# Kernel optimization log

Hardware: AMD Instinct MI355X
Metric: run time of the kernel (lower is better)

The kernel has to match this reference:

```python
import jax, jax.numpy as jnp
import numpy as np

N = 100000      # nodes
E = 3200000     # edges (avg degree 32)
IN_CH = 32
EDGE_DIM = 11
HID = IN_CH + 4 + EDGE_DIM   # 47
OUT = 128


def setup_inputs() -> dict:
    key = jax.random.key(0)
    ks = jax.random.split(key, 10)
    x = jax.random.normal(ks[0], (N, IN_CH), dtype=jnp.float32)
    pos = jax.random.normal(ks[1], (N, 3), dtype=jnp.float32) * 10.0
    nrm = jax.random.normal(ks[2], (N, 3), dtype=jnp.float32)
    normal = nrm / jnp.linalg.norm(nrm, axis=1, keepdims=True)
    # edges with src != dst (avoids degenerate zero-distance point pairs)
    src = jax.random.randint(ks[3], (E,), 0, N)
    off = jax.random.randint(ks[4], (E,), 1, N)
    dst = (src + off) % N
    edge_index = jnp.stack([src, dst], axis=0).astype(jnp.int64)
    edge_attr = jax.random.normal(ks[5], (E, EDGE_DIM), dtype=jnp.float32)
    W1 = jax.random.normal(ks[6], (HID, HID), dtype=jnp.float32) / np.sqrt(HID)
    b1 = jnp.zeros((HID,), dtype=jnp.float32)
    g1 = jnp.ones((HID,), dtype=jnp.float32)
    be1 = jnp.zeros((HID,), dtype=jnp.float32)
    W2 = jax.random.normal(ks[7], (HID, OUT), dtype=jnp.float32) / np.sqrt(HID)
    b2 = jnp.zeros((OUT,), dtype=jnp.float32)
    g2 = jnp.ones((OUT,), dtype=jnp.float32)
    be2 = jnp.zeros((OUT,), dtype=jnp.float32)
    return {"x": x, "pos": pos, "normal": normal, "edge_attr": edge_attr,
            "W1": W1, "b1": b1, "g1": g1, "be1": be1,
            "W2": W2, "b2": b2, "g2": g2, "be2": be2,
            "edge_index": edge_index}


def _angle(v1, v2):
    return jnp.arctan2(jnp.linalg.norm(jnp.cross(v1, v2), axis=1),
                       jnp.sum(v1 * v2, axis=1))


def _layernorm(h, g, b, eps=1e-5):
    mu = jnp.mean(h, axis=-1, keepdims=True)
    var = jnp.var(h, axis=-1, keepdims=True)  # biased, matches torch LayerNorm
    return (h - mu) / jnp.sqrt(var + eps) * g + b


def reference(x, pos, normal, edge_attr, W1, b1, g1, be1, W2, b2, g2, be2, edge_index):
    src, dst = edge_index[0], edge_index[1]  # message flows src(j) -> dst(i)
    pos_i, pos_j = pos[dst], pos[src]
    n_i, n_j = normal[dst], normal[src]
    x_j = x[src]
    pseudo = pos_j - pos_i                                  # [E,3]
    ppf = jnp.stack([jnp.linalg.norm(pseudo, axis=1),
                     _angle(n_i, pseudo),
                     _angle(n_j, pseudo),
                     _angle(n_i, n_j)], axis=1)             # [E,4]
    msg = jnp.concatenate([x_j, ppf, edge_attr], axis=1)    # [E,47]
    # local_nn = MLP([47,47,128]): (Lin->ReLU->LayerNorm->Dropout(eval)) x2
    h = _layernorm(jax.nn.relu(msg @ W1 + b1), g1, be1)     # [E,47]
    h = _layernorm(jax.nn.relu(h @ W2 + b2), g2, be2)       # [E,128]
    out = jax.ops.segment_max(h, dst, num_segments=N)       # scatter-max per target node
    return jnp.where(jnp.isfinite(out), out, 0.0)           # nodes w/o edges -> 0
```

## Files before the change

kernel.cpp:

```cpp
#include <hip/hip_runtime.h>
#include <cstdint>
#include <cstddef>


typedef _Float16 f16x8 __attribute__((ext_vector_type(8)));
typedef _Float16 f16x2 __attribute__((ext_vector_type(2)));
typedef float    f32x4 __attribute__((ext_vector_type(4)));

#define ENC_NEGINF 0x007FFFFFu
#define LDK 64
#define LDH 132

__device__ __forceinline__ int swz(int row, int col) {
    return (col & 7) | ((((col >> 3) ^ row) & 7) << 3);
}

__device__ __forceinline__ unsigned fenc(float f) {
    unsigned u = __float_as_uint(f);
    return (u & 0x80000000u) ? ~u : (u | 0x80000000u);
}

__device__ __forceinline__ float fdec(unsigned k) {
    if (k == ENC_NEGINF) return 0.0f;
    unsigned u = (k & 0x80000000u) ? (k ^ 0x80000000u) : ~k;
    return __uint_as_float(u);
}

__device__ __forceinline__ f16x2 pkrtz(float a, float b) {
    auto p = __builtin_amdgcn_cvt_pkrtz(a, b);
    return __builtin_bit_cast(f16x2, p);
}

__global__ void init_out_kernel(unsigned* __restrict__ out, int n4) {
    int i = blockIdx.x * blockDim.x + threadIdx.x;
    if (i < n4)
        ((uint4*)out)[i] = make_uint4(ENC_NEGINF, ENC_NEGINF, ENC_NEGINF, ENC_NEGINF);
}

__global__ void finalize_out_kernel(float* __restrict__ out, int n4) {
    int i = blockIdx.x * blockDim.x + threadIdx.x;
    if (i < n4) {
        uint4 k = ((const uint4*)out)[i];
        float4 r;
        r.x = fdec(k.x); r.y = fdec(k.y); r.z = fdec(k.z); r.w = fdec(k.w);
        ((float4*)out)[i] = r;
    }
}

__global__ void hist_kernel(const int* __restrict__ dstI, int* __restrict__ counts, int E) {
    int i = blockIdx.x * blockDim.x + threadIdx.x;
    if (i < E) atomicAdd(&counts[dstI[i]], 1);
}

__global__ __launch_bounds__(1024) void scan_blk(const int* __restrict__ in,
                                                 int* __restrict__ outp,
                                                 int* __restrict__ bsums, int N) {
    __shared__ int wsum[16];
    const int tid = threadIdx.x, lane = tid & 63, wid = tid >> 6;
    int i = blockIdx.x * 1024 + tid;
    int v = (i < N) ? in[i] : 0;
    int incl = v;
#pragma unroll
    for (int m = 1; m < 64; m <<= 1) {
        int t = __shfl_up(incl, m, 64);
        if (lane >= m) incl += t;
    }
    if (lane == 63) wsum[wid] = incl;
    __syncthreads();
    int woff = 0;
#pragma unroll
    for (int k = 0; k < 16; ++k) woff += (k < wid) ? wsum[k] : 0;
    if (i < N) outp[i] = woff + incl - v;
    if (tid == 1023 && bsums != nullptr) bsums[blockIdx.x] = woff + incl;
}

__global__ void scatter_kernel(const int* __restrict__ srcI, const int* __restrict__ dstI,
                               int* __restrict__ nextp, const int* __restrict__ bsums,
                               int2* __restrict__ se, int* __restrict__ dst_g, int E) {
    int i = blockIdx.x * blockDim.x + threadIdx.x;
    if (i < E) {
        int d = dstI[i];
        int p = bsums[d >> 10] + atomicAdd(&nextp[d], 1);
        se[p] = make_int2(srcI[i], i);
        dst_g[p] = d;
    }
}

__global__ __launch_bounds__(512, 4) void edge_kernel_csr(
    const float* __restrict__ x,   const float* __restrict__ pos,
    const float* __restrict__ nrm, const float* __restrict__ ea,
    const float* __restrict__ W1,  const float* __restrict__ b1,
    const float* __restrict__ g1,  const float* __restrict__ be1,
    const float* __restrict__ W2,  const float* __restrict__ b2,
    const float* __restrict__ g2,  const float* __restrict__ be2,
    const int2* __restrict__ se,   const int* __restrict__ dst_g,
    unsigned* __restrict__ out, int E, int ntiles, int tilesPerBlock)
{
    __shared__ _Float16 W1t[48][LDK];
    __shared__ _Float16 W2t[128][LDK];
    __shared__ _Float16 msgA[128][LDK];
    __shared__ _Float16 h2w[128][LDH];
    __shared__ int dstL[128];

    const int lane = threadIdx.x & 63;
    const int w    = threadIdx.x >> 6;
    const int c16  = lane & 15;
    const int g    = lane >> 4;
    const int row0 = w * 16;

    for (int i = threadIdx.x; i < 48 * 64; i += 512) {
        int n = i >> 6, k = i & 63;
        W1t[n][swz(n, k)] = (n < 47 && k < 47) ? (_Float16)W1[k * 47 + n] : (_Float16)0.f;
    }
    for (int i = threadIdx.x; i < 128 * 64; i += 512) {
        int n = i >> 6, k = i & 63;
        W2t[n][swz(n, k)] = (k < 47) ? (_Float16)W2[k * 128 + n] : (_Float16)0.f;
    }
    for (int i = threadIdx.x; i < 128 * LDK; i += 512)
        (&msgA[0][0])[i] = (_Float16)0.f;

    float b1v[3], g1v[3], be1v[3];
#pragma unroll
    for (int n = 0; n < 3; ++n) {
        int cc = n * 16 + c16;
        bool vld = cc < 47;
        b1v[n]  = vld ? b1[cc]  : 0.f;
        g1v[n]  = vld ? g1[cc]  : 0.f;
        be1v[n] = vld ? be1[cc] : 0.f;
    }
    float b2v[8];
    f16x2 g2pk[4], be2pk[4];
#pragma unroll
    for (int n = 0; n < 8; ++n) b2v[n] = b2[n * 16 + c16];
#pragma unroll
    for (int h = 0; h < 4; ++h) {
        g2pk[h][0]  = (_Float16)g2[(2 * h) * 16 + c16];
        g2pk[h][1]  = (_Float16)g2[(2 * h + 1) * 16 + c16];
        be2pk[h][0] = (_Float16)be2[(2 * h) * 16 + c16];
        be2pk[h][1] = (_Float16)be2[(2 * h + 1) * 16 + c16];
    }
    __syncthreads();

    const int xr = lane >> 2;
    const int xc = (lane & 3) * 8;
    const int eg = lane / 11, ec = lane - eg * 11;
    const bool ea_act  = lane < 44;
    const bool geo_act = lane < 48;

    const int tbeg = blockIdx.x * tilesPerBlock;
    int tend = tbeg + tilesPerBlock;
    if (tend > ntiles) tend = ntiles;
    if (tbeg >= tend) return;

    int   pf_sx = 0;
    int   pf_e0 = -1, pf_e1 = -1, pf_e2 = -1, pf_e3 = -1;
    int   pf_gs = 0,  pf_gd = -1;
    float pf_ea0 = 0.f, pf_ea1 = 0.f, pf_ea2 = 0.f, pf_ea3 = 0.f;

    {
        const int b2 = tbeg * 128 + row0;
        int p = b2 + xr;
        pf_sx = (p < E) ? se[p].x : 0;
        if (ea_act) {
            int p0 = b2 + eg, p1 = b2 + 4 + eg, p2 = b2 + 8 + eg, p3 = b2 + 12 + eg;
            pf_e0 = (p0 < E) ? se[p0].y : -1;
            pf_e1 = (p1 < E) ? se[p1].y : -1;
            pf_e2 = (p2 < E) ? se[p2].y : -1;
            pf_e3 = (p3 < E) ? se[p3].y : -1;
            pf_ea0 = (pf_e0 >= 0) ? ea[(size_t)pf_e0 * 11 + ec] : 0.f;
            pf_ea1 = (pf_e1 >= 0) ? ea[(size_t)pf_e1 * 11 + ec] : 0.f;
            pf_ea2 = (pf_e2 >= 0) ? ea[(size_t)pf_e2 * 11 + ec] : 0.f;
            pf_ea3 = (pf_e3 >= 0) ? ea[(size_t)pf_e3 * 11 + ec] : 0.f;
        }
        if (geo_act) {
            int pg = b2 + c16;
            bool v = pg < E;
            pf_gs = v ? se[pg].x : 0;
            pf_gd = v ? dst_g[pg] : -1;
        }
    }

    for (int tile = tbeg; tile < tend; ++tile) {
        const int base = tile * 128 + row0;
        const bool more = (tile + 1 < tend);

        const int   c_sx  = pf_sx;
        const int   c_gs  = pf_gs;
        const int   c_gd  = pf_gd;
        const float cea0 = pf_ea0, cea1 = pf_ea1, cea2 = pf_ea2, cea3 = pf_ea3;

        if (more) {
            const int b2 = base + 128;
            int p = b2 + xr;
            pf_sx = (p < E) ? se[p].x : 0;
            if (ea_act) {
                int p0 = b2 + eg, p1 = b2 + 4 + eg, p2 = b2 + 8 + eg, p3 = b2 + 12 + eg;
                pf_e0 = (p0 < E) ? se[p0].y : -1;
                pf_e1 = (p1 < E) ? se[p1].y : -1;
                pf_e2 = (p2 < E) ? se[p2].y : -1;
                pf_e3 = (p3 < E) ? se[p3].y : -1;
            }
            if (geo_act) {
                int pg = b2 + c16;
                bool v = pg < E;
                pf_gs = v ? se[pg].x : 0;
                pf_gd = v ? dst_g[pg] : -1;
            }
        }

        {
            int p = base + xr;
            bool vx = p < E;
            const float4* xp = (const float4*)(x + (size_t)c_sx * 32 + xc);
            float4 xa = xp[0];
            float4 xb = xp[1];

            float gpix = 0.f, gpiy = 0.f, gpiz = 0.f;
            float gpjx = 0.f, gpjy = 0.f, gpjz = 0.f;
            float gnix = 0.f, gniy = 0.f, gniz = 0.f;
            float gnjx = 0.f, gnjy = 0.f, gnjz = 0.f;
            if (geo_act) {
                int d2 = (c_gd < 0) ? 0 : c_gd;
                gpix = pos[d2 * 3 + 0]; gpiy = pos[d2 * 3 + 1]; gpiz = pos[d2 * 3 + 2];
                gpjx = pos[c_gs * 3 + 0]; gpjy = pos[c_gs * 3 + 1]; gpjz = pos[c_gs * 3 + 2];
                gnix = nrm[d2 * 3 + 0]; gniy = nrm[d2 * 3 + 1]; gniz = nrm[d2 * 3 + 2];
                gnjx = nrm[c_gs * 3 + 0]; gnjy = nrm[c_gs * 3 + 1]; gnjz = nrm[c_gs * 3 + 2];
            }

            {
                int r = row0 + xr;
                f16x8 hv;
                hv[0] = (_Float16)(vx ? xa.x : 0.f); hv[1] = (_Float16)(vx ? xa.y : 0.f);
                hv[2] = (_Float16)(vx ? xa.z : 0.f); hv[3] = (_Float16)(vx ? xa.w : 0.f);
                hv[4] = (_Float16)(vx ? xb.x : 0.f); hv[5] = (_Float16)(vx ? xb.y : 0.f);
                hv[6] = (_Float16)(vx ? xb.z : 0.f); hv[7] = (_Float16)(vx ? xb.w : 0.f);
                *(f16x8*)&msgA[r][swz(r, xc)] = hv;
            }
            if (ea_act) {
                int r0 = row0 + 0 * 4 + eg; msgA[r0][swz(r0, 36 + ec)] = (_Float16)cea0;
                int r1 = row0 + 1 * 4 + eg; msgA[r1][swz(r1, 36 + ec)] = (_Float16)cea1;
                int r2 = row0 + 2 * 4 + eg; msgA[r2][swz(r2, 36 + ec)] = (_Float16)cea2;
                int r3 = row0 + 3 * 4 + eg; msgA[r3][swz(r3, 36 + ec)] = (_Float16)cea3;
            }
            if (geo_act) {
                int r = row0 + c16;
                float px = gpjx - gpix, py = gpjy - gpiy, pz = gpjz - gpiz;
                float v1x, v1y, v1z, v2x, v2y, v2z;
                if (g == 0)      { v1x = gnix; v1y = gniy; v1z = gniz; v2x = px;   v2y = py;   v2z = pz; }
                else if (g == 1) { v1x = gnjx; v1y = gnjy; v1z = gnjz; v2x = px;   v2y = py;   v2z = pz; }
                else             { v1x = gnix; v1y = gniy; v1z = gniz; v2x = gnjx; v2y = gnjy; v2z = gnjz; }
                float cx = v1y * v2z - v1z * v2y;
                float cy = v1z * v2x - v1x * v2z;
                float cz = v1x * v2y - v1y * v2x;
                float ang = atan2f(sqrtf(cx * cx + cy * cy + cz * cz),
                                   v1x * v2x + v1y * v2y + v1z * v2z);
                msgA[r][swz(r, 33 + g)] = (_Float16)ang;
                if (g == 0) {
                    msgA[r][swz(r, 32)] = (_Float16)sqrtf(px * px + py * py + pz * pz);
                    dstL[r] = c_gd;
                }
            }
        }

        f32x4 acc1[3];
#pragma unroll
        for (int n = 0; n < 3; ++n) acc1[n] = (f32x4){0.f, 0.f, 0.f, 0.f};
#pragma unroll
        for (int ks = 0; ks < 2; ++ks) {
            int ar = row0 + c16;
            f16x8 a = *(const f16x8*)&msgA[ar][swz(ar, ks * 32 + g * 8)];
#pragma unroll
            for (int n = 0; n < 3; ++n) {
                int br = n * 16 + c16;
                f16x8 b = *(const f16x8*)&W1t[br][swz(br, ks * 32 + g * 8)];
                acc1[n] = __builtin_amdgcn_mfma_f32_16x16x32_f16(a, b, acc1[n], 0, 0, 0);
            }
        }
#pragma unroll
        for (int q = 0; q < 4; ++q) {
            float t0 = fmaxf(acc1[0][q] + b1v[0], 0.f);
            float t1 = fmaxf(acc1[1][q] + b1v[1], 0.f);
            float t2 = fmaxf(acc1[2][q] + b1v[2], 0.f);
            float s = t0 + t1 + t2;
            float s2 = t0 * t0 + t1 * t1 + t2 * t2;
#pragma unroll
            for (int m = 1; m < 16; m <<= 1) {
                s  += __shfl_xor(s,  m, 64);
                s2 += __shfl_xor(s2, m, 64);
            }
            float mu  = s * (1.f / 47.f);
            float var = s2 * (1.f / 47.f) - mu * mu;
            float rs  = rsqrtf(var + 1e-5f);
            int r = row0 + 4 * g + q;
            msgA[r][swz(r, c16)]      = (_Float16)((t0 - mu) * rs * g1v[0] + be1v[0]);
            msgA[r][swz(r, 16 + c16)] = (_Float16)((t1 - mu) * rs * g1v[1] + be1v[1]);
            msgA[r][swz(r, 32 + c16)] = (_Float16)((t2 - mu) * rs * g1v[2] + be1v[2]);
        }

        if (more && ea_act) {
            pf_ea0 = (pf_e0 >= 0) ? ea[(size_t)pf_e0 * 11 + ec] : 0.f;
            pf_ea1 = (pf_e1 >= 0) ? ea[(size_t)pf_e1 * 11 + ec] : 0.f;
            pf_ea2 = (pf_e2 >= 0) ? ea[(size_t)pf_e2 * 11 + ec] : 0.f;
            pf_ea3 = (pf_e3 >= 0) ? ea[(size_t)pf_e3 * 11 + ec] : 0.f;
        }

        f32x4 acc2[8];
#pragma unroll
        for (int n = 0; n < 8; ++n) acc2[n] = (f32x4){0.f, 0.f, 0.f, 0.f};
#pragma unroll
        for (int ks = 0; ks < 2; ++ks) {
            int ar = row0 + c16;
            f16x8 a = *(const f16x8*)&msgA[ar][swz(ar, ks * 32 + g * 8)];
#pragma unroll
            for (int n = 0; n < 8; ++n) {
                int br = n * 16 + c16;
                f16x8 b = *(const f16x8*)&W2t[br][swz(br, ks * 32 + g * 8)];
                acc2[n] = __builtin_amdgcn_mfma_f32_16x16x32_f16(a, b, acc2[n], 0, 0, 0);
            }
        }
#pragma unroll
        for (int q = 0; q < 4; ++q) {
            float t[8];
            float s = 0.f, s2 = 0.f;
#pragma unroll
            for (int n = 0; n < 8; ++n) {
                t[n] = fmaxf(acc2[n][q] + b2v[n], 0.f);
                s += t[n]; s2 += t[n] * t[n];
            }
#pragma unroll
            for (int m = 1; m < 16; m <<= 1) {
                s  += __shfl_xor(s,  m, 64);
                s2 += __shfl_xor(s2, m, 64);
            }
            float mu  = s * (1.f / 128.f);
            float var = s2 * (1.f / 128.f) - mu * mu;
            float rs  = rsqrtf(var + 1e-5f);
            int r = row0 + 4 * g + q;
            f16x2 apk = pkrtz(rs, rs);
            f16x2 cpk = pkrtz(-mu * rs, -mu * rs);
#pragma unroll
            for (int h = 0; h < 4; ++h) {
                f16x2 tpk = pkrtz(t[2 * h], t[2 * h + 1]);
                f16x2 z   = tpk * apk + cpk;
                f16x2 hvp = z * g2pk[h] + be2pk[h];
                h2w[r][(2 * h) * 16 + c16]     = hvp[0];
                h2w[r][(2 * h + 1) * 16 + c16] = hvp[1];
            }
        }

        {
            f16x2 mneg; mneg[0] = mneg[1] = (_Float16)(-65504.f);
            f16x2 mx = mneg;
            int segStart = 0;
            int dcur = dstL[row0];
#pragma unroll
            for (int r = 0; r < 16; ++r) {
                f16x2 pk = *(const f16x2*)&h2w[row0 + r][lane * 2];
                mx[0] = (pk[0] > mx[0]) ? pk[0] : mx[0];
                mx[1] = (pk[1] > mx[1]) ? pk[1] : mx[1];
                int dnext = (r < 15) ? dstL[row0 + r + 1] : -2;
                if (dnext != dcur) {
                    if (dcur >= 0) {
                        unsigned e0 = fenc((float)mx[0]);
                        unsigned e1 = fenc((float)mx[1]);
                        unsigned* orow = out + (size_t)dcur * 128 + lane * 2;
                        if (segStart > 0 && r < 15) {
                            unsigned long long pk2 =
                                ((unsigned long long)e1 << 32) | (unsigned long long)e0;
                            *(unsigned long long*)orow = pk2;
                        } else {
                            atomicMax(orow,     e0);
                            atomicMax(orow + 1, e1);
                        }
                    }
                    mx = mneg;
                    segStart = r + 1; dcur = dnext;
                }
            }
        }
    }
}

#define LDKF 72
__global__ __launch_bounds__(256) void edge_kernel_atomic(
    const float* __restrict__ x,   const float* __restrict__ pos,
    const float* __restrict__ nrm, const float* __restrict__ ea,
    const float* __restrict__ W1,  const float* __restrict__ b1,
    const float* __restrict__ g1,  const float* __restrict__ be1,
    const float* __restrict__ W2,  const float* __restrict__ b2,
    const float* __restrict__ g2,  const float* __restrict__ be2,
    const int* __restrict__ srcI,  const int* __restrict__ dstI,
    unsigned* __restrict__ out, int E, int ntiles)
{
    __shared__ _Float16 W1t[48][LDKF];
    __shared__ _Float16 W2t[128][LDKF];
    __shared__ _Float16 msgA[64][LDKF];
    __shared__ int dst_s[64];

    const int lane = threadIdx.x & 63;
    const int w    = threadIdx.x >> 6;
    const int c16  = lane & 15;
    const int g    = lane >> 4;

    for (int i = threadIdx.x; i < 48 * 64; i += 256) {
        int n = i >> 6, k = i & 63;
        W1t[n][k] = (n < 47 && k < 47) ? (_Float16)W1[k * 47 + n] : (_Float16)0.f;
    }
    for (int i = threadIdx.x; i < 128 * 64; i += 256) {
        int n = i >> 6, k = i & 63;
        W2t[n][k] = (k < 47) ? (_Float16)W2[k * 128 + n] : (_Float16)0.f;
    }
    for (int i = threadIdx.x; i < 64 * LDKF; i += 256)
        (&msgA[0][0])[i] = (_Float16)0.f;

    float b1v[3], g1v[3], be1v[3];
#pragma unroll
    for (int n = 0; n < 3; ++n) {
        int cc = n * 16 + c16;
        bool vld = cc < 47;
        b1v[n]  = vld ? b1[cc]  : 0.f;
        g1v[n]  = vld ? g1[cc]  : 0.f;
        be1v[n] = vld ? be1[cc] : 0.f;
    }
    float b2v[8], g2v[8], be2v[8];
#pragma unroll
    for (int n = 0; n < 8; ++n) {
        int cc = n * 16 + c16;
        b2v[n] = b2[cc]; g2v[n] = g2[cc]; be2v[n] = be2[cc];
    }
    __syncthreads();

    for (int tile = blockIdx.x; tile < ntiles; tile += gridDim.x) {
        const int base = tile * 64 + w * 16;
        const int row0 = w * 16;
#pragma unroll
        for (int i = 0; i < 8; ++i) {
            int el = i * 2 + (lane >> 5);
            int e  = base + el;
            int c  = lane & 31;
            float v = 0.f;
            if (e < E) v = x[(size_t)srcI[e] * 32 + c];
            msgA[row0 + el][c] = (_Float16)v;
        }
        if (lane < 44) {
            int eg = lane / 11, c = lane - eg * 11;
#pragma unroll
            for (int i = 0; i < 4; ++i) {
                int el = i * 4 + eg;
                int e  = base + el;
                float v = 0.f;
                if (e < E) v = ea[(size_t)e * 11 + c];
                msgA[row0 + el][36 + c] = (_Float16)v;
            }
        }
        if (lane < 48) {
            int el = c16;
            int e  = base + el;
            int s = 0, d = 0;
            bool vld = e < E;
            if (vld) { s = srcI[e]; d = dstI[e]; }
            float pix = pos[d * 3 + 0], piy = pos[d * 3 + 1], piz = pos[d * 3 + 2];
            float pjx = pos[s * 3 + 0], pjy = pos[s * 3 + 1], pjz = pos[s * 3 + 2];
            float nix = nrm[d * 3 + 0], niy = nrm[d * 3 + 1], niz = nrm[d * 3 + 2];
            float njx = nrm[s * 3 + 0], njy = nrm[s * 3 + 1], njz = nrm[s * 3 + 2];
            float px = pjx - pix, py = pjy - piy, pz = pjz - piz;
            float v1x, v1y, v1z, v2x, v2y, v2z;
            if (g == 0)      { v1x = nix; v1y = niy; v1z = niz; v2x = px;  v2y = py;  v2z = pz;  }
            else if (g == 1) { v1x = njx; v1y = njy; v1z = njz; v2x = px;  v2y = py;  v2z = pz;  }
            else             { v1x = nix; v1y = niy; v1z = niz; v2x = njx; v2y = njy; v2z = njz; }
            float cx = v1y * v2z - v1z * v2y;
            float cy = v1z * v2x - v1x * v2z;
            float cz = v1x * v2y - v1y * v2x;
            float ang = atan2f(sqrtf(cx * cx + cy * cy + cz * cz),
                               v1x * v2x + v1y * v2y + v1z * v2z);
            msgA[row0 + el][33 + g] = (_Float16)ang;
            if (g == 0) {
                msgA[row0 + el][32] = (_Float16)sqrtf(px * px + py * py + pz * pz);
                dst_s[row0 + el] = vld ? d : -1;
            }
        }

        f32x4 acc1[3];
#pragma unroll
        for (int n = 0; n < 3; ++n) acc1[n] = (f32x4){0.f, 0.f, 0.f, 0.f};
#pragma unroll
        for (int ks = 0; ks < 2; ++ks) {
            f16x8 a = *(const f16x8*)&msgA[row0 + c16][ks * 32 + g * 8];
#pragma unroll
            for (int n = 0; n < 3; ++n) {
                f16x8 b = *(const f16x8*)&W1t[n * 16 + c16][ks * 32 + g * 8];
                acc1[n] = __builtin_amdgcn_mfma_f32_16x16x32_f16(a, b, acc1[n], 0, 0, 0);
            }
        }
#pragma unroll
        for (int q = 0; q < 4; ++q) {
            float t0 = fmaxf(acc1[0][q] + b1v[0], 0.f);
            float t1 = fmaxf(acc1[1][q] + b1v[1], 0.f);
            float t2 = fmaxf(acc1[2][q] + b1v[2], 0.f);
            float s = t0 + t1 + t2;
            float s2 = t0 * t0 + t1 * t1 + t2 * t2;
#pragma unroll
            for (int m = 1; m < 16; m <<= 1) {
                s  += __shfl_xor(s,  m, 64);
                s2 += __shfl_xor(s2, m, 64);
            }
            float mu  = s * (1.f / 47.f);
            float var = s2 * (1.f / 47.f) - mu * mu;
            float rs  = rsqrtf(var + 1e-5f);
            int r = row0 + 4 * g + q;
            msgA[r][c16]      = (_Float16)((t0 - mu) * rs * g1v[0] + be1v[0]);
            msgA[r][16 + c16] = (_Float16)((t1 - mu) * rs * g1v[1] + be1v[1]);
            msgA[r][32 + c16] = (_Float16)((t2 - mu) * rs * g1v[2] + be1v[2]);
        }

        f32x4 acc2[8];
#pragma unroll
        for (int n = 0; n < 8; ++n) acc2[n] = (f32x4){0.f, 0.f, 0.f, 0.f};
#pragma unroll
        for (int ks = 0; ks < 2; ++ks) {
            f16x8 a = *(const f16x8*)&msgA[row0 + c16][ks * 32 + g * 8];
#pragma unroll
            for (int n = 0; n < 8; ++n) {
                f16x8 b = *(const f16x8*)&W2t[n * 16 + c16][ks * 32 + g * 8];
                acc2[n] = __builtin_amdgcn_mfma_f32_16x16x32_f16(a, b, acc2[n], 0, 0, 0);
            }
        }
        int4 dd = *(const int4*)&dst_s[row0 + 4 * g];
#pragma unroll
        for (int q = 0; q < 4; ++q) {
            float t[8];
            float s = 0.f, s2 = 0.f;
#pragma unroll
            for (int n = 0; n < 8; ++n) {
                t[n] = fmaxf(acc2[n][q] + b2v[n], 0.f);
                s += t[n]; s2 += t[n] * t[n];
            }
#pragma unroll
            for (int m = 1; m < 16; m <<= 1) {
                s  += __shfl_xor(s,  m, 64);
                s2 += __shfl_xor(s2, m, 64);
            }
            float mu  = s * (1.f / 128.f);
            float var = s2 * (1.f / 128.f) - mu * mu;
            float rs  = rsqrtf(var + 1e-5f);
            int d = (&dd.x)[q];
            if (d >= 0) {
                unsigned* orow = out + (size_t)d * 128u;
#pragma unroll
                for (int n = 0; n < 8; ++n) {
                    float o = (t[n] - mu) * rs * g2v[n] + be2v[n];
                    atomicMax(orow + n * 16 + c16, fenc(o));
                }
            }
        }
    }
}

extern "C" void kernel_launch(void* const* d_in, const int* in_sizes, int n_in,
                              void* d_out, int out_size, void* d_ws, size_t ws_size,
                              hipStream_t stream) {
    const float* x   = (const float*)d_in[0];
    const float* pos = (const float*)d_in[1];
    const float* nrm = (const float*)d_in[2];
    const float* ea  = (const float*)d_in[3];
    const float* W1  = (const float*)d_in[4];
    const float* b1  = (const float*)d_in[5];
    const float* g1  = (const float*)d_in[6];
    const float* be1 = (const float*)d_in[7];
    const float* W2  = (const float*)d_in[8];
    const float* b2  = (const float*)d_in[9];
    const float* g2  = (const float*)d_in[10];
    const float* be2 = (const float*)d_in[11];
    const int*   idx = (const int*)d_in[12];

    const int N = in_sizes[0] / 32;
    const int E = in_sizes[3] / 11;
    const int* srcI = idx;
    const int* dstI = idx + E;

    unsigned* outU = (unsigned*)d_out;
    const int n = N * 128;

    init_out_kernel<<<(n / 4 + 255) / 256, 256, 0, stream>>>(outU, n / 4);

    const int nb = (N + 1023) / 1024;
    const size_t needed = (size_t)E * 8 + (size_t)(2LL * N + E + nb) * 4;

    if (ws_size >= needed) {
        int2* se     = (int2*)d_ws;
        int*  counts = (int*)(se + E);
        int*  nextp  = counts + N;
        int*  dst_g  = nextp + N;
        int*  bsums  = dst_g + E;

        hipMemsetAsync(counts, 0, (size_t)N * 4, stream);
        hist_kernel<<<(E + 255) / 256, 256, 0, stream>>>(dstI, counts, E);
        scan_blk<<<nb, 1024, 0, stream>>>(counts, nextp, bsums, N);
        scan_blk<<<1, 1024, 0, stream>>>(bsums, bsums, (int*)nullptr, nb);
        scatter_kernel<<<(E + 255) / 256, 256, 0, stream>>>(srcI, dstI, nextp, bsums,
                                                            se, dst_g, E);

        const int ntiles = (E + 127) / 128;
        int grid = ntiles < 512 ? ntiles : 512;
        int tpb  = (ntiles + grid - 1) / grid;
        edge_kernel_csr<<<grid, 512, 0, stream>>>(x, pos, nrm, ea,
                                                  W1, b1, g1, be1,
                                                  W2, b2, g2, be2,
                                                  se, dst_g,
                                                  outU, E, ntiles, tpb);
    } else {
        const int ntiles = (E + 63) / 64;
        int grid = ntiles < 4096 ? ntiles : 4096;
        edge_kernel_atomic<<<grid, 256, 0, stream>>>(x, pos, nrm, ea,
                                                     W1, b1, g1, be1,
                                                     W2, b2, g2, be2,
                                                     srcI, dstI, outU, E, ntiles);
    }

    finalize_out_kernel<<<(n / 4 + 255) / 256, 256, 0, stream>>>((float*)d_out, n / 4);
}
```

Before: 842.3 us.

## Prefetch x rows a tile ahead, precompute swizzled offsets, ballot segment boundaries

The x-row gather for the next tile is now issued together with the edge-attribute prefetch, one tile ahead, so the message build for the current tile uses values already in registers. That build moves ahead of the next-tile index prefetch, and pos/normal are read as 3-float vectors. Swizzled LDS offsets for the MFMA operand loads are computed once outside the loop, and the per-row segment-boundary checks in the scatter-max are replaced by a single ballot mask. The cost is more live registers for the prefetched x data, which may lower occupancy.

```diff
diff --git a/kernel.cpp b/kernel.cpp
--- a/kernel.cpp
+++ b/kernel.cpp
@@ -6,6 +6,7 @@
 typedef _Float16 f16x8 __attribute__((ext_vector_type(8)));
 typedef _Float16 f16x2 __attribute__((ext_vector_type(2)));
 typedef float    f32x4 __attribute__((ext_vector_type(4)));
+typedef float    f32x3 __attribute__((ext_vector_type(3)));
 
 #define ENC_NEGINF 0x007FFFFFu
 #define LDK 64
@@ -147,15 +148,24 @@
     const bool ea_act  = lane < 44;
     const bool geo_act = lane < 48;
 
+    const int x7   = c16 & 7;
+    const int k0off = ((0 + g) ^ x7) * 16;
+    const int k1off = ((4 + g) ^ x7) * 16;
+    const char* aRow  = (const char*)&msgA[row0 + c16][0];
+    const char* w1Row = (const char*)&W1t[c16][0];
+    const char* w2Row = (const char*)&W2t[c16][0];
+
     const int tbeg = blockIdx.x * tilesPerBlock;
     int tend = tbeg + tilesPerBlock;
     if (tend > ntiles) tend = ntiles;
     if (tbeg >= tend) return;
 
-    int   pf_sx = 0;
-    int   pf_e0 = -1, pf_e1 = -1, pf_e2 = -1, pf_e3 = -1;
-    int   pf_gs = 0,  pf_gd = -1;
-    float pf_ea0 = 0.f, pf_ea1 = 0.f, pf_ea2 = 0.f, pf_ea3 = 0.f;
+    int    pf_sx = 0;
+    int    pf_e0 = -1, pf_e1 = -1, pf_e2 = -1, pf_e3 = -1;
+    int    pf_gs = 0,  pf_gd = -1;
+    float  pf_ea0 = 0.f, pf_ea1 = 0.f, pf_ea2 = 0.f, pf_ea3 = 0.f;
+    float4 pf_xa = make_float4(0.f, 0.f, 0.f, 0.f);
+    float4 pf_xb = make_float4(0.f, 0.f, 0.f, 0.f);
 
     {
         const int b2 = tbeg * 128 + row0;
@@ -167,10 +177,6 @@
             pf_e1 = (p1 < E) ? se[p1].y : -1;
             pf_e2 = (p2 < E) ? se[p2].y : -1;
             pf_e3 = (p3 < E) ? se[p3].y : -1;
-            pf_ea0 = (pf_e0 >= 0) ? ea[(size_t)pf_e0 * 11 + ec] : 0.f;
-            pf_ea1 = (pf_e1 >= 0) ? ea[(size_t)pf_e1 * 11 + ec] : 0.f;
-            pf_ea2 = (pf_e2 >= 0) ? ea[(size_t)pf_e2 * 11 + ec] : 0.f;
-            pf_ea3 = (pf_e3 >= 0) ? ea[(size_t)pf_e3 * 11 + ec] : 0.f;
         }
         if (geo_act) {
             int pg = b2 + c16;
@@ -178,16 +184,61 @@
             pf_gs = v ? se[pg].x : 0;
             pf_gd = v ? dst_g[pg] : -1;
         }
+        const float4* xp = (const float4*)(x + (pf_sx * 32 + xc));
+        pf_xa = xp[0]; pf_xb = xp[1];
+        if (ea_act) {
+            pf_ea0 = (pf_e0 >= 0) ? ea[pf_e0 * 11 + ec] : 0.f;
+            pf_ea1 = (pf_e1 >= 0) ? ea[pf_e1 * 11 + ec] : 0.f;
+            pf_ea2 = (pf_e2 >= 0) ? ea[pf_e2 * 11 + ec] : 0.f;
+            pf_ea3 = (pf_e3 >= 0) ? ea[pf_e3 * 11 + ec] : 0.f;
+        }
     }
 
     for (int tile = tbeg; tile < tend; ++tile) {
         const int base = tile * 128 + row0;
         const bool more = (tile + 1 < tend);
 
-        const int   c_sx  = pf_sx;
-        const int   c_gs  = pf_gs;
-        const int   c_gd  = pf_gd;
-        const float cea0 = pf_ea0, cea1 = pf_ea1, cea2 = pf_ea2, cea3 = pf_ea3;
+        {
+            bool vx = (base + xr) < E;
+            {
+                int r = row0 + xr;
+                f16x8 hv;
+                hv[0] = (_Float16)(vx ? pf_xa.x : 0.f); hv[1] = (_Float16)(vx ? pf_xa.y : 0.f);
+                hv[2] = (_Float16)(vx ? pf_xa.z : 0.f); hv[3] = (_Float16)(vx ? pf_xa.w : 0.f);
+                hv[4] = (_Float16)(vx ? pf_xb.x : 0.f); hv[5] = (_Float16)(vx ? pf_xb.y : 0.f);
+                hv[6] = (_Float16)(vx ? pf_xb.z : 0.f); hv[7] = (_Float16)(vx ? pf_xb.w : 0.f);
+                *(f16x8*)&msgA[r][swz(r, xc)] = hv;
+            }
+            if (ea_act) {
+                int r0 = row0 + 0 * 4 + eg; msgA[r0][swz(r0, 36 + ec)] = (_Float16)pf_ea0;
+                int r1 = row0 + 1 * 4 + eg; msgA[r1][swz(r1, 36 + ec)] = (_Float16)pf_ea1;
+                int r2 = row0 + 2 * 4 + eg; msgA[r2][swz(r2, 36 + ec)] = (_Float16)pf_ea2;
+                int r3 = row0 + 3 * 4 + eg; msgA[r3][swz(r3, 36 + ec)] = (_Float16)pf_ea3;
+            }
+            if (geo_act) {
+                int d2 = (pf_gd < 0) ? 0 : pf_gd;
+                f32x3 pi = *(const f32x3*)(pos + 3 * d2);
+                f32x3 pj = *(const f32x3*)(pos + 3 * pf_gs);
+                f32x3 ni = *(const f32x3*)(nrm + 3 * d2);
+                f32x3 nj = *(const f32x3*)(nrm + 3 * pf_gs);
+                int r = row0 + c16;
+                float px = pj[0] - pi[0], py = pj[1] - pi[1], pz = pj[2] - pi[2];
+                float v1x, v1y, v1z, v2x, v2y, v2z;
+                if (g == 0)      { v1x = ni[0]; v1y = ni[1]; v1z = ni[2]; v2x = px;    v2y = py;    v2z = pz; }
+                else if (g == 1) { v1x = nj[0]; v1y = nj[1]; v1z = nj[2]; v2x = px;    v2y = py;    v2z = pz; }
+                else             { v1x = ni[0]; v1y = ni[1]; v1z = ni[2]; v2x = nj[0]; v2y = nj[1]; v2z = nj[2]; }
+                float cx = v1y * v2z - v1z * v2y;
+                float cy = v1z * v2x - v1x * v2z;
+                float cz = v1x * v2y - v1y * v2x;
+                float ang = atan2f(sqrtf(cx * cx + cy * cy + cz * cz),
+                                   v1x * v2x + v1y * v2y + v1z * v2z);
+                msgA[r][swz(r, 33 + g)] = (_Float16)ang;
+                if (g == 0) {
+                    msgA[r][swz(r, 32)] = (_Float16)sqrtf(px * px + py * py + pz * pz);
+                    dstL[r] = pf_gd;
+                }
+            }
+        }
 
         if (more) {
             const int b2 = base + 128;
@@ -208,72 +259,18 @@
             }
         }
 
+        f32x4 acc1[3];
+#pragma unroll
+        for (int n = 0; n < 3; ++n) acc1[n] = (f32x4){0.f, 0.f, 0.f, 0.f};
         {
-            int p = base + xr;
-            bool vx = p < E;
-            const float4* xp = (const float4*)(x + (size_t)c_sx * 32 + xc);
-            float4 xa = xp[0];
-            float4 xb = xp[1];
-
-            float gpix = 0.f, gpiy = 0.f, gpiz = 0.f;
-            float gpjx = 0.f, gpjy = 0.f, gpjz = 0.f;
-            float gnix = 0.f, gniy = 0.f, gniz = 0.f;
-            float gnjx = 0.f, gnjy = 0.f, gnjz = 0.f;
-            if (geo_act) {
-                int d2 = (c_gd < 0) ? 0 : c_gd;
-                gpix = pos[d2 * 3 + 0]; gpiy = pos[d2 * 3 + 1]; gpiz = pos[d2 * 3 + 2];
-                gpjx = pos[c_gs * 3 + 0]; gpjy = pos[c_gs * 3 + 1]; gpjz = pos[c_gs * 3 + 2];
-                gnix = nrm[d2 * 3 + 0]; gniy = nrm[d2 * 3 + 1]; gniz = nrm[d2 * 3 + 2];
-                gnjx = nrm[c_gs * 3 + 0]; gnjy = nrm[c_gs * 3 + 1]; gnjz = nrm[c_gs * 3 + 2];
-            }
-
-            {
-                int r = row0 + xr;
-                f16x8 hv;
-                hv[0] = (_Float16)(vx ? xa.x : 0.f); hv[1] = (_Float16)(vx ? xa.y : 0.f);
-                hv[2] = (_Float16)(vx ? xa.z : 0.f); hv[3] = (_Float16)(vx ? xa.w : 0.f);
-                hv[4] = (_Float16)(vx ? xb.x : 0.f); hv[5] = (_Float16)(vx ? xb.y : 0.f);
-                hv[6] = (_Float16)(vx ? xb.z : 0.f); hv[7] = (_Float16)(vx ? xb.w : 0.f);
-                *(f16x8*)&msgA[r][swz(r, xc)] = hv;
-            }
-            if (ea_act) {
-                int r0 = row0 + 0 * 4 + eg; msgA[r0][swz(r0, 36 + ec)] = (_Float16)cea0;
-                int r1 = row0 + 1 * 4 + eg; msgA[r1][swz(r1, 36 + ec)] = (_Float16)cea1;
-                int r2 = row0 + 2 * 4 + eg; msgA[r2][swz(r2, 36 + ec)] = (_Float16)cea2;
-                int r3 = row0 + 3 * 4 + eg; msgA[r3][swz(r3, 36 + ec)] = (_Float16)cea3;
-            }
-            if (geo_act) {
-                int r = row0 + c16;
-                float px = gpjx - gpix, py = gpjy - gpiy, pz = gpjz - gpiz;
-                float v1x, v1y, v1z, v2x, v2y, v2z;
-                if (g == 0)      { v1x = gnix; v1y = gniy; v1z = gniz; v2x = px;   v2y = py;   v2z = pz; }
-                else if (g == 1) { v1x = gnjx; v1y = gnjy; v1z = gnjz; v2x = px;   v2y = py;   v2z = pz; }
-                else             { v1x = gnix; v1y = gniy; v1z = gniz; v2x = gnjx; v2y = gnjy; v2z = gnjz; }
-                float cx = v1y * v2z - v1z * v2y;
-                float cy = v1z * v2x - v1x * v2z;
-                float cz = v1x * v2y - v1y * v2x;
-                float ang = atan2f(sqrtf(cx * cx + cy * cy + cz * cz),
-                                   v1x * v2x + v1y * v2y + v1z * v2z);
-                msgA[r][swz(r, 33 + g)] = (_Float16)ang;
-                if (g == 0) {
-                    msgA[r][swz(r, 32)] = (_Float16)sqrtf(px * px + py * py + pz * pz);
-                    dstL[r] = c_gd;
-                }
-            }
-        }
-
-        f32x4 acc1[3];
-#pragma unroll
-        for (int n = 0; n < 3; ++n) acc1[n] = (f32x4){0.f, 0.f, 0.f, 0.f};
-#pragma unroll
-        for (int ks = 0; ks < 2; ++ks) {
-            int ar = row0 + c16;
-            f16x8 a = *(const f16x8*)&msgA[ar][swz(ar, ks * 32 + g * 8)];
+            f16x8 a0 = *(const f16x8*)(aRow + k0off);
+            f16x8 a1 = *(const f16x8*)(aRow + k1off);
 #pragma unroll
             for (int n = 0; n < 3; ++n) {
-                int br = n * 16 + c16;
-                f16x8 b = *(const f16x8*)&W1t[br][swz(br, ks * 32 + g * 8)];
-                acc1[n] = __builtin_amdgcn_mfma_f32_16x16x32_f16(a, b, acc1[n], 0, 0, 0);
+                f16x8 b0 = *(const f16x8*)(w1Row + n * 2048 + k0off);
+                f16x8 b1 = *(const f16x8*)(w1Row + n * 2048 + k1off);
+                acc1[n] = __builtin_amdgcn_mfma_f32_16x16x32_f16(a0, b0, acc1[n], 0, 0, 0);
+                acc1[n] = __builtin_amdgcn_mfma_f32_16x16x32_f16(a1, b1, acc1[n], 0, 0, 0);
             }
         }
 #pragma unroll
@@ -297,25 +294,29 @@
             msgA[r][swz(r, 32 + c16)] = (_Float16)((t2 - mu) * rs * g1v[2] + be1v[2]);
         }
 
-        if (more && ea_act) {
-            pf_ea0 = (pf_e0 >= 0) ? ea[(size_t)pf_e0 * 11 + ec] : 0.f;
-            pf_ea1 = (pf_e1 >= 0) ? ea[(size_t)pf_e1 * 11 + ec] : 0.f;
-            pf_ea2 = (pf_e2 >= 0) ? ea[(size_t)pf_e2 * 11 + ec] : 0.f;
-            pf_ea3 = (pf_e3 >= 0) ? ea[(size_t)pf_e3 * 11 + ec] : 0.f;
+        if (more) {
+            const float4* xp = (const float4*)(x + (pf_sx * 32 + xc));
+            pf_xa = xp[0]; pf_xb = xp[1];
+            if (ea_act) {
+                pf_ea0 = (pf_e0 >= 0) ? ea[pf_e0 * 11 + ec] : 0.f;
+                pf_ea1 = (pf_e1 >= 0) ? ea[pf_e1 * 11 + ec] : 0.f;
+                pf_ea2 = (pf_e2 >= 0) ? ea[pf_e2 * 11 + ec] : 0.f;
+                pf_ea3 = (pf_e3 >= 0) ? ea[pf_e3 * 11 + ec] : 0.f;
+            }
         }
 
         f32x4 acc2[8];
 #pragma unroll
         for (int n = 0; n < 8; ++n) acc2[n] = (f32x4){0.f, 0.f, 0.f, 0.f};
-#pragma unroll
-        for (int ks = 0; ks < 2; ++ks) {
-            int ar = row0 + c16;
-            f16x8 a = *(const f16x8*)&msgA[ar][swz(ar, ks * 32 + g * 8)];
+        {
+            f16x8 a0 = *(const f16x8*)(aRow + k0off);
+            f16x8 a1 = *(const f16x8*)(aRow + k1off);
 #pragma unroll
             for (int n = 0; n < 8; ++n) {
-                int br = n * 16 + c16;
-                f16x8 b = *(const f16x8*)&W2t[br][swz(br, ks * 32 + g * 8)];
-                acc2[n] = __builtin_amdgcn_mfma_f32_16x16x32_f16(a, b, acc2[n], 0, 0, 0);
+                f16x8 b0 = *(const f16x8*)(w2Row + n * 2048 + k0off);
+                f16x8 b1 = *(const f16x8*)(w2Row + n * 2048 + k1off);
+                acc2[n] = __builtin_amdgcn_mfma_f32_16x16x32_f16(a0, b0, acc2[n], 0, 0, 0);
+                acc2[n] = __builtin_amdgcn_mfma_f32_16x16x32_f16(a1, b1, acc2[n], 0, 0, 0);
             }
         }
 #pragma unroll
@@ -349,17 +350,23 @@
         }
 
         {
+            unsigned long long bmask;
+            {
+                int rr = lane & 15;
+                int dc = dstL[row0 + rr];
+                int dn = (rr < 15) ? dstL[row0 + rr + 1] : -2;
+                bmask = __ballot(lane < 16 && dc != dn) | (1ull << 15);
+            }
             f16x2 mneg; mneg[0] = mneg[1] = (_Float16)(-65504.f);
             f16x2 mx = mneg;
             int segStart = 0;
-            int dcur = dstL[row0];
 #pragma unroll
             for (int r = 0; r < 16; ++r) {
                 f16x2 pk = *(const f16x2*)&h2w[row0 + r][lane * 2];
                 mx[0] = (pk[0] > mx[0]) ? pk[0] : mx[0];
                 mx[1] = (pk[1] > mx[1]) ? pk[1] : mx[1];
-                int dnext = (r < 15) ? dstL[row0 + r + 1] : -2;
-                if (dnext != dcur) {
+                if ((bmask >> r) & 1) {
+                    int dcur = dstL[row0 + r];
                     if (dcur >= 0) {
                         unsigned e0 = fenc((float)mx[0]);
                         unsigned e1 = fenc((float)mx[1]);
@@ -374,7 +381,7 @@
                         }
                     }
                     mx = mneg;
-                    segStart = r + 1; dcur = dnext;
+                    segStart = r + 1;
                 }
             }
         }
```

New measurement: 1.027 ms. +21.9%, slower.
